# Performance work log

Measured on AMD Instinct MI355X. Metric: run time of the kernel, lower is better.

The kernel has to match this reference:

```python
import jax, jax.numpy as jnp
import numpy as np

B, GNN_DIM, TR_DIM, F = 16384, 512, 768, 1024


def setup_inputs() -> dict:
    key = jax.random.key(0)
    ks = jax.random.split(key, 16)
    s = 0.02
    return {
        "gnn_features": jax.random.normal(ks[0], (B, GNN_DIM), jnp.float32),
        "transformer_features": jax.random.normal(ks[1], (B, TR_DIM), jnp.float32),
        # gnn_projector / transformer_projector (torch Linear: y = x @ W.T + b)
        "Wg": jax.random.normal(ks[2], (F, GNN_DIM), jnp.float32) * s,
        "bg": jnp.zeros((F,), jnp.float32),
        "Wt": jax.random.normal(ks[3], (F, TR_DIM), jnp.float32) * s,
        "bt": jnp.zeros((F,), jnp.float32),
        # MultiheadAttention value-projection slice of in_proj_weight and out_proj.
        # With seq_len==1 the softmax over a single key is identically 1, so the
        # attention output is exactly out_proj(v_proj(key)); Q/K projections do
        # not affect the output (their gradients are exactly zero).
        "Wv": jax.random.normal(ks[4], (F, F), jnp.float32) * s,
        "bv": jnp.zeros((F,), jnp.float32),
        "Wo": jax.random.normal(ks[5], (F, F), jnp.float32) * s,
        "bo": jnp.zeros((F,), jnp.float32),
        # fusion_layers: Linear(2F -> F), GELU, Dropout(eval: identity), Linear(F -> F)
        "W1": jax.random.normal(ks[6], (F, 2 * F), jnp.float32) * s,
        "b1": jnp.zeros((F,), jnp.float32),
        "W2": jax.random.normal(ks[7], (F, F), jnp.float32) * s,
        "b2": jnp.zeros((F,), jnp.float32),
    }


def reference(gnn_features, transformer_features, Wg, bg, Wt, bt, Wv, bv, Wo, bo, W1, b1, W2, b2):
    # projections to fusion space  [B, F]
    gnn_proj = gnn_features @ Wg.T + bg
    tr_proj = transformer_features @ Wt.T + bt
    # degenerate single-token cross-attention: softmax over 1 key == 1, so
    # attn(q, k, v=k) = out_proj(v_proj(k)) regardless of the query.
    gnn_attended = (tr_proj @ Wv.T + bv) @ Wo.T + bo   # attention(gnn_seq, tr_seq, tr_seq)
    tr_attended = (gnn_proj @ Wv.T + bv) @ Wo.T + bo   # attention(tr_seq, gnn_seq, gnn_seq)
    combined = jnp.concatenate([gnn_attended, tr_attended], axis=-1)  # [B, 2F]
    h = jax.nn.gelu(combined @ W1.T + b1, approximate=False)          # exact GELU (torch default)
    fused = h @ W2.T + b2
    return fused + gnn_proj + tr_proj
```

## Files before the change

### kernel.cpp

```cpp
#include <hip/hip_runtime.h>
#include <cmath>

#define GAS __attribute__((address_space(1)))
#define LAS __attribute__((address_space(3)))

typedef __bf16 bf16x8 __attribute__((ext_vector_type(8)));
typedef float f32x4 __attribute__((ext_vector_type(4)));
typedef float f32x16 __attribute__((ext_vector_type(16)));

__device__ __forceinline__ void gload16(const void* g, void* l) {
    __builtin_amdgcn_global_load_lds((const GAS void*)g, (LAS void*)l, 16, 0, 0);
}

__global__ void k_prep(const float* __restrict__ gnn, const float* __restrict__ tr,
                       const float* __restrict__ Wo, const float* __restrict__ W1,
                       const float* __restrict__ W2, const float* __restrict__ Wg,
                       const float* __restrict__ Wt, const float* __restrict__ Wv,
                       __bf16* __restrict__ X, __bf16* __restrict__ W1ab,
                       __bf16* __restrict__ Wp, __bf16* __restrict__ Wv_b,
                       __bf16* __restrict__ WoT, __bf16* __restrict__ WgT,
                       __bf16* __restrict__ WtT) {
    __shared__ float t[32][33];
    int b = blockIdx.x;
    int tid = threadIdx.x;
    if (b < 12928) {
        const float* src; __bf16* dst; int sld, dld, base, c8;
        if (b < 4096)       { src=gnn;     sld=512;  dst=X+1024;         dld=2304; base=0;     c8=64; }
        else if (b < 10240) { src=tr;      sld=768;  dst=X+1536;         dld=2304; base=4096;  c8=96; }
        else if (b < 10752) { src=W1;      sld=2048; dst=W1ab;           dld=1024; base=10240; c8=128; }
        else if (b < 11264) { src=W1+1024; sld=2048; dst=W1ab+1024*1024; dld=1024; base=10752; c8=128; }
        else if (b < 11776) { src=W2;      sld=1024; dst=Wp;             dld=2304; base=11264; c8=128; }
        else if (b < 12032) { src=Wg;      sld=512;  dst=Wp+1024;        dld=2304; base=11776; c8=64; }
        else if (b < 12416) { src=Wt;      sld=768;  dst=Wp+1536;        dld=2304; base=12032; c8=96; }
        else                { src=Wv;      sld=1024; dst=Wv_b;           dld=1024; base=12416; c8=128; }
        int idx = (b - base) * 256 + tid;
        int r = idx / c8;
        int c = (idx - r * c8) << 3;
        const float4* s = reinterpret_cast<const float4*>(src + (long)r * sld + c);
        float4 x0 = s[0], x1 = s[1];
        bf16x8 v;
        v[0]=(__bf16)x0.x; v[1]=(__bf16)x0.y; v[2]=(__bf16)x0.z; v[3]=(__bf16)x0.w;
        v[4]=(__bf16)x1.x; v[5]=(__bf16)x1.y; v[6]=(__bf16)x1.z; v[7]=(__bf16)x1.w;
        *reinterpret_cast<bf16x8*>(dst + (long)r * dld + c) = v;
    } else {
        int bb = b - 12928;
        const float* src; __bf16* dst; int R, C, tile;
        if (bb < 1024)      { src=Wo; dst=WoT; R=1024; C=1024; tile=bb; }
        else if (bb < 1536) { src=Wg; dst=WgT; R=1024; C=512;  tile=bb-1024; }
        else                { src=Wt; dst=WtT; R=1024; C=768;  tile=bb-1536; }
        int tx_n = C >> 5;
        int c0 = (tile % tx_n) << 5, r0 = (tile / tx_n) << 5;
        int tx = tid & 31, ty = tid >> 5;
        #pragma unroll
        for (int i = 0; i < 32; i += 8)
            t[ty + i][tx] = src[(long)(r0 + ty + i) * C + c0 + tx];
        __syncthreads();
        #pragma unroll
        for (int i = 0; i < 32; i += 8)
            dst[(long)(c0 + ty + i) * R + r0 + tx] = (__bf16)t[tx][ty + i];
    }
}

__global__ void k_bias1(const float* __restrict__ Wo, const float* __restrict__ bv,
                        const float* __restrict__ bo, const float* __restrict__ Wv,
                        const float* __restrict__ bt, const float* __restrict__ bg,
                        float* __restrict__ b_att, float* __restrict__ vb_t,
                        float* __restrict__ vb_g) {
    int b = blockIdx.x;
    const float* mat; const float* vec; float* dst; int i; bool addbo = false;
    if (b < 1024)      { mat = Wo; vec = bv; dst = b_att; i = b;        addbo = true; }
    else if (b < 2048) { mat = Wv; vec = bt; dst = vb_t;  i = b - 1024; }
    else               { mat = Wv; vec = bg; dst = vb_g;  i = b - 2048; }
    float s = 0.f;
    for (int k = threadIdx.x; k < 1024; k += 256) s += mat[(long)i * 1024 + k] * vec[k];
    __shared__ float red[256];
    red[threadIdx.x] = s;
    __syncthreads();
    for (int off = 128; off > 0; off >>= 1) {
        if (threadIdx.x < off) red[threadIdx.x] += red[threadIdx.x + off];
        __syncthreads();
    }
    if (threadIdx.x == 0) dst[i] = red[0] + (addbo ? bo[i] : 0.f);
}

__global__ void k_bias_z2(const float* __restrict__ W1, const float* __restrict__ b_att,
                          const float* __restrict__ b1, const __bf16* __restrict__ U12,
                          const float* __restrict__ vb_t, const float* __restrict__ vb_g,
                          const float* __restrict__ bt, const float* __restrict__ bg,
                          const float* __restrict__ b2,
                          float* __restrict__ bz2, float* __restrict__ b_out) {
    int i = blockIdx.x;
    float s = 0.f;
    for (int k = threadIdx.x; k < 1024; k += 256) {
        s += (W1[(long)i * 2048 + k] + W1[(long)i * 2048 + 1024 + k]) * b_att[k];
        s += (float)U12[(long)i * 1024 + k] * vb_t[k];
        s += (float)U12[(long)(i + 1024) * 1024 + k] * vb_g[k];
    }
    __shared__ float red[256];
    red[threadIdx.x] = s;
    __syncthreads();
    for (int off = 128; off > 0; off >>= 1) {
        if (threadIdx.x < off) red[threadIdx.x] += red[threadIdx.x + off];
        __syncthreads();
    }
    if (threadIdx.x == 0) {
        bz2[i] = red[0] + b1[i];
        b_out[i] = b2[i] + bg[i] + bt[i];
    }
}

__device__ __forceinline__ void gemm64_body(
    const __bf16* __restrict__ A, int lda,
    const __bf16* __restrict__ B, int ldb,
    __bf16* __restrict__ C, int ldc,
    int K, int n_tiles, int bid) {
    constexpr int BM = 64, BN = 64, BK = 32;
    constexpr int MR = 2, NR = 2;
    __shared__ alignas(16) __bf16 As[2][BM][BK];
    __shared__ alignas(16) __bf16 Bs[2][BN][BK];

    const int tid = threadIdx.x;
    const int lane = tid & 63;
    const int wave = tid >> 6;
    const int bn = bid % n_tiles;
    const int bm = bid / n_tiles;
    const int m0 = bm * BM, n0 = bn * BN;

    const int rp_l = tid >> 2;
    const int sp = tid & 3;
    const int wr = (wave >> 1) * 32;
    const int wc = (wave & 1) * 32;
    const int fr = lane & 15;
    const int fb = (lane >> 4) << 4;

    f32x4 acc[MR][NR] = {};
    const int nk = K / BK;

    auto stage = [&](int buf, int kt) {
        int rl = (rp_l & ~1) | ((rp_l ^ (rp_l >> 2)) & 1);
        int sl = sp ^ (rl & 3);
        gload16(A + (long)(m0 + rl) * lda + kt * BK + sl * 8, (char*)&As[buf][0][0] + tid * 16);
        gload16(B + (long)(n0 + rl) * ldb + kt * BK + sl * 8, (char*)&Bs[buf][0][0] + tid * 16);
    };

    stage(0, 0);
    for (int kt = 0; kt < nk; ++kt) {
        const int buf = kt & 1;
        __syncthreads();
        if (kt + 1 < nk) stage(buf ^ 1, kt + 1);
        const char* abase = (const char*)&As[buf][0][0];
        const char* bbase = (const char*)&Bs[buf][0][0];
        bf16x8 af[MR], bfr[NR];
        #pragma unroll
        for (int m = 0; m < MR; ++m) {
            int r = wr + m * 16 + fr;
            af[m] = *(const bf16x8*)(abase + (((r << 6) + fb) ^ ((r & 7) << 4)));
        }
        #pragma unroll
        for (int n = 0; n < NR; ++n) {
            int r = wc + n * 16 + fr;
            bfr[n] = *(const bf16x8*)(bbase + (((r << 6) + fb) ^ ((r & 7) << 4)));
        }
        #pragma unroll
        for (int m = 0; m < MR; ++m)
            #pragma unroll
            for (int n = 0; n < NR; ++n)
                acc[m][n] = __builtin_amdgcn_mfma_f32_16x16x32_bf16(af[m], bfr[n], acc[m][n], 0, 0, 0);
    }

    const int r0 = (lane >> 4) << 2;
    #pragma unroll
    for (int n = 0; n < NR; ++n) {
        const int gc = n0 + wc + n * 16 + fr;
        #pragma unroll
        for (int m = 0; m < MR; ++m) {
            const long rbase = (long)(m0 + wr + m * 16 + r0);
            #pragma unroll
            for (int r = 0; r < 4; ++r)
                C[(rbase + r) * ldc + gc] = (__bf16)acc[m][n][r];
        }
    }
}

__global__ __launch_bounds__(256, 2) void k_gemmL1(
    const __bf16* __restrict__ W1ab, const __bf16* __restrict__ WoT,
    const __bf16* __restrict__ WtT, const __bf16* __restrict__ WgT,
    const __bf16* __restrict__ Wv_b, __bf16* __restrict__ U12,
    __bf16* __restrict__ VtT, __bf16* __restrict__ VgT) {
    int b = blockIdx.x;
    if (b < 512)      gemm64_body(W1ab, 1024, WoT, 1024, U12, 1024, 1024, 16, b);
    else if (b < 704) gemm64_body(WtT, 1024, Wv_b, 1024, VtT, 1024, 1024, 16, b - 512);
    else              gemm64_body(WgT, 1024, Wv_b, 1024, VgT, 1024, 1024, 16, b - 704);
}

__global__ __launch_bounds__(256, 2) void k_gemmL2(
    const __bf16* __restrict__ U12, const __bf16* __restrict__ VtT,
    const __bf16* __restrict__ VgT, __bf16* __restrict__ M1) {
    int b = blockIdx.x;
    if (b < 192) gemm64_body(U12, 1024, VtT, 1024, M1 + 512, 1280, 1024, 12, b);
    else         gemm64_body(U12 + 1024 * 1024, 1024, VgT, 1024, M1, 1280, 1024, 8, b - 192);
}

template <int MODE>
__device__ __forceinline__ void gemm8_body(
    const __bf16* __restrict__ A, int lda,
    const __bf16* __restrict__ B, int ldb,
    void* __restrict__ Cv, int ldc,
    const float* __restrict__ bias,
    int K, int n_tiles) {
    __shared__ char lds[131072];

    const int tid = threadIdx.x;
    const int lane = tid & 63;
    const int wave = tid >> 6;
    const int wm = wave >> 2;
    const int wn = wave & 3;

    int bid = blockIdx.x;
    const int nwg = gridDim.x;
    if ((nwg & 7) == 0) bid = (bid & 7) * (nwg >> 3) + (bid >> 3);
    const int bn = bid % n_tiles;
    const int bm = bid / n_tiles;
    const int m0 = bm * 256, n0 = bn * 256;

    const int rowA = ((tid >> 7) << 4) + (tid & 15);
    const int colA = (((tid >> 6) & 1) << 5) + (((tid >> 4) & 3) << 3);
    const int rowB = ((tid >> 6) << 4) + (tid & 15);
    const int colB = (((tid >> 4) & 3) << 3);
    const __bf16* Ag = A + (long)(m0 + rowA) * lda + colA;
    const __bf16* Bg = B + (long)(n0 + rowB) * ldb + colB;
    const int tid16 = tid * 16;

    const int laneA = ((lane >> 4) & 1) * 2048 + (lane >> 5) * 256 + (lane & 15) * 16;
    const int laneB = ((lane >> 4) & 1) * 1024 + (lane >> 5) * 256 + (lane & 15) * 16;
    const int bnh = wn >> 1;
    const int bno = (wn & 1) * 4096;

    f32x16 acc[4][2] = {};
    bf16x8 af[2][2];
    bf16x8 bfr[2][2][2];

    const int nk = K >> 6;
    const int NI = nk >> 1;

#define STAGE_A(PAR, KT, MH, QH) \
    gload16(Ag + (long)(KT) * 64 + (long)((MH) * 128 + (QH) * 64) * lda, \
            lds + (PAR) * 32768 + (MH) * 16384 + (QH) * 8192 + tid16)
#define STAGE_B(PAR, KT, NH, KK) \
    gload16(Bg + (long)(KT) * 64 + (KK) * 32 + (long)((NH) * 128) * ldb, \
            lds + 65536 + (PAR) * 32768 + (NH) * 16384 + (KK) * 8192 + tid16)
#define VMC8 asm volatile("s_waitcnt vmcnt(8)" ::: "memory")
#define VMC6 asm volatile("s_waitcnt vmcnt(6)" ::: "memory")
#define VMC0 asm volatile("s_waitcnt vmcnt(0)" ::: "memory")
#define BAR  __builtin_amdgcn_s_barrier()
#define RD_A32(PAR, QH, KK) { \
        const char* a_ = lds + (PAR) * 32768 + wm * 16384 + (QH) * 8192 + (KK) * 1024; \
        _Pragma("unroll") \
        for (int fm_ = 0; fm_ < 2; ++fm_) { \
            _Pragma("unroll") \
            for (int h_ = 0; h_ < 2; ++h_) \
                af[fm_][h_] = *(const bf16x8*)(a_ + fm_ * 4096 + h_ * 512 + laneA); } }
#define RD_B32(KK, PAR) { \
        const char* b_ = lds + 65536 + (PAR) * 32768 + bnh * 16384 + (KK) * 8192 + bno; \
        _Pragma("unroll") \
        for (int fn_ = 0; fn_ < 2; ++fn_) { \
            _Pragma("unroll") \
            for (int h_ = 0; h_ < 2; ++h_) \
                bfr[KK][h_][fn_] = *(const bf16x8*)(b_ + fn_ * 2048 + h_ * 512 + laneB); } }
#define MFMA8(QH, KK) { \
        __builtin_amdgcn_s_setprio(1); \
        _Pragma("unroll") \
        for (int h_ = 0; h_ < 2; ++h_) { \
            _Pragma("unroll") \
            for (int fm_ = 0; fm_ < 2; ++fm_) { \
                _Pragma("unroll") \
                for (int fn_ = 0; fn_ < 2; ++fn_) \
                    acc[(QH) * 2 + fm_][fn_] = __builtin_amdgcn_mfma_f32_32x32x16_bf16( \
                        af[fm_][h_], bfr[KK][h_][fn_], acc[(QH) * 2 + fm_][fn_], 0, 0, 0); } } \
        __builtin_amdgcn_s_setprio(0); }

    STAGE_A(0, 0, 0, 0); STAGE_A(0, 0, 1, 0);
    STAGE_B(0, 0, 0, 0); STAGE_B(0, 0, 1, 0);
    STAGE_A(0, 0, 0, 1); STAGE_A(0, 0, 1, 1);
    STAGE_B(0, 0, 0, 1); STAGE_B(0, 0, 1, 1);
    STAGE_A(1, 1, 0, 0); STAGE_A(1, 1, 1, 0);
    STAGE_B(1, 1, 0, 0); STAGE_B(1, 1, 1, 0);

    for (int I = 0; I < NI; ++I) {
        const int t = 2 * I;
        const bool nl = (I + 1 < NI);
        VMC8;
        STAGE_A(1, t + 1, 0, 1); STAGE_A(1, t + 1, 1, 1);
        BAR; RD_B32(0, 0); RD_A32(0, 0, 0); MFMA8(0, 0); BAR;
        VMC6;
        STAGE_B(1, t + 1, 0, 1); STAGE_B(1, t + 1, 1, 1);
        BAR; RD_B32(1, 0); RD_A32(0, 0, 1); MFMA8(0, 1); BAR;
        if (nl) { STAGE_A(0, t + 2, 0, 0); STAGE_A(0, t + 2, 1, 0); } else { VMC0; }
        BAR; RD_A32(0, 1, 0); MFMA8(1, 0); BAR;
        if (nl) { STAGE_B(0, t + 2, 0, 0); STAGE_B(0, t + 2, 1, 0); }
        BAR; RD_A32(0, 1, 1); MFMA8(1, 1); BAR;
        VMC8;
        if (nl) { STAGE_A(0, t + 2, 0, 1); STAGE_A(0, t + 2, 1, 1); }
        BAR; RD_B32(0, 1); RD_A32(1, 0, 0); MFMA8(0, 0); BAR;
        VMC6;
        if (nl) { STAGE_B(0, t + 2, 0, 1); STAGE_B(0, t + 2, 1, 1); }
        BAR; RD_B32(1, 1); RD_A32(1, 0, 1); MFMA8(0, 1); BAR;
        if (nl) { STAGE_A(1, t + 3, 0, 0); STAGE_A(1, t + 3, 1, 0); }
        BAR; RD_A32(1, 1, 0); MFMA8(1, 0); BAR;
        if (nl) { STAGE_B(1, t + 3, 0, 0); STAGE_B(1, t + 3, 1, 0); }
        BAR; RD_A32(1, 1, 1); MFMA8(1, 1); BAR;
    }
#undef MFMA8
#undef RD_B32
#undef RD_A32
#undef BAR
#undef VMC0
#undef VMC6
#undef VMC8
#undef STAGE_B
#undef STAGE_A

    char* scr = lds + wave * 16384;
    const int col32 = lane & 31;
    const int rb5 = (lane >> 5) << 2;
    float bval[2];
    bval[0] = bias ? bias[n0 + wn * 64 + col32] : 0.0f;
    bval[1] = bias ? bias[n0 + wn * 64 + 32 + col32] : 0.0f;

    #pragma unroll
    for (int FM = 0; FM < 4; ++FM) {
        #pragma unroll
        for (int fn_ = 0; fn_ < 2; ++fn_) {
            #pragma unroll
            for (int rg = 0; rg < 16; ++rg) {
                float v = acc[FM][fn_][rg] + bval[fn_];
                if (MODE == 1) {
                    float u = v * (0.7978845608f + 0.0356774081f * v * v);
                    float e = __expf(-2.0f * fabsf(u));
                    float th = (1.0f - e) / (1.0f + e);
                    th = copysignf(th, u);
                    v = 0.5f * v * (1.0f + th);
                }
                int srow = (rg & 3) + ((rg >> 2) << 3) + rb5;
                *(float*)(scr + srow * 272 + (fn_ * 32 + col32) * 4) = v;
            }
        }
        asm volatile("s_waitcnt lgkmcnt(0)" ::: "memory");
        if (MODE == 2) {
            #pragma unroll
            for (int rep = 0; rep < 8; ++rep) {
                int row = rep * 4 + (lane >> 4);
                f32x4 val = *(const f32x4*)(scr + row * 272 + (lane & 15) * 16);
                long grow = (long)(m0 + wm * 128 + FM * 32 + row);
                *(f32x4*)&((float*)Cv)[grow * ldc + n0 + wn * 64 + (lane & 15) * 4] = val;
            }
        } else {
            #pragma unroll
            for (int rep = 0; rep < 4; ++rep) {
                int row = rep * 8 + (lane >> 3);
                f32x4 v0 = *(const f32x4*)(scr + row * 272 + (lane & 7) * 32);
                f32x4 v1 = *(const f32x4*)(scr + row * 272 + (lane & 7) * 32 + 16);
                bf16x8 o;
                o[0] = (__bf16)v0[0]; o[1] = (__bf16)v0[1]; o[2] = (__bf16)v0[2]; o[3] = (__bf16)v0[3];
                o[4] = (__bf16)v1[0]; o[5] = (__bf16)v1[1]; o[6] = (__bf16)v1[2]; o[7] = (__bf16)v1[3];
                long grow = (long)(m0 + wm * 128 + FM * 32 + row);
                *(bf16x8*)&((__bf16*)Cv)[grow * ldc + n0 + wn * 64 + (lane & 7) * 8] = o;
            }
        }
        asm volatile("s_waitcnt lgkmcnt(0)" ::: "memory");
    }
}

__global__ __launch_bounds__(512, 2) void k_g256_gelu(
    const __bf16* __restrict__ A, int lda, const __bf16* __restrict__ B, int ldb,
    void* __restrict__ Cv, int ldc, const float* __restrict__ bias, int K, int n_tiles) {
    gemm8_body<1>(A, lda, B, ldb, Cv, ldc, bias, K, n_tiles);
}
__global__ __launch_bounds__(512, 2) void k_g256_out(
    const __bf16* __restrict__ A, int lda, const __bf16* __restrict__ B, int ldb,
    void* __restrict__ Cv, int ldc, const float* __restrict__ bias, int K, int n_tiles) {
    gemm8_body<2>(A, lda, B, ldb, Cv, ldc, bias, K, n_tiles);
}

extern "C" void kernel_launch(void* const* d_in, const int* in_sizes, int n_in,
                              void* d_out, int out_size, void* d_ws, size_t ws_size,
                              hipStream_t stream) {
    constexpr int Bsz = 16384, F = 1024, GD = 512, TD = 768;
    constexpr int XLD = F + GD + TD;

    const float* gnn = (const float*)d_in[0];
    const float* tr  = (const float*)d_in[1];
    const float* Wg  = (const float*)d_in[2];
    const float* bg  = (const float*)d_in[3];
    const float* Wt  = (const float*)d_in[4];
    const float* bt  = (const float*)d_in[5];
    const float* Wv  = (const float*)d_in[6];
    const float* bv  = (const float*)d_in[7];
    const float* Wo  = (const float*)d_in[8];
    const float* bo  = (const float*)d_in[9];
    const float* W1  = (const float*)d_in[10];
    const float* b1  = (const float*)d_in[11];
    const float* W2  = (const float*)d_in[12];
    const float* b2  = (const float*)d_in[13];
    float* out = (float*)d_out;

    char* w = (char*)d_ws;
    auto alloc = [&](size_t bytes) {
        char* p = w;
        w += (bytes + 255) & ~(size_t)255;
        return p;
    };
    __bf16* X    = (__bf16*)alloc((size_t)Bsz * XLD * 2);
    __bf16* M1   = (__bf16*)alloc((size_t)F * (GD + TD) * 2);
    __bf16* Wp   = (__bf16*)alloc((size_t)F * XLD * 2);
    __bf16* W1ab = (__bf16*)alloc((size_t)2 * F * F * 2);
    __bf16* Wv_b = (__bf16*)alloc((size_t)F * F * 2);
    __bf16* WoT  = (__bf16*)alloc((size_t)F * F * 2);
    __bf16* WgT  = (__bf16*)alloc((size_t)GD * F * 2);
    __bf16* WtT  = (__bf16*)alloc((size_t)TD * F * 2);
    __bf16* U12  = (__bf16*)alloc((size_t)2 * F * F * 2);
    __bf16* VtT  = (__bf16*)alloc((size_t)TD * F * 2);
    __bf16* VgT  = (__bf16*)alloc((size_t)GD * F * 2);
    float* b_att = (float*)alloc(F * 4);
    float* vb_t  = (float*)alloc(F * 4);
    float* vb_g  = (float*)alloc(F * 4);
    float* bz2   = (float*)alloc(F * 4);
    float* b_out = (float*)alloc(F * 4);
    if ((size_t)(w - (char*)d_ws) > ws_size) return;

    dim3 b256(256);

    k_prep<<<dim3(15232), b256, 0, stream>>>(gnn, tr, Wo, W1, W2, Wg, Wt, Wv,
                                             X, W1ab, Wp, Wv_b, WoT, WgT, WtT);
    k_bias1<<<dim3(3072), b256, 0, stream>>>(Wo, bv, bo, Wv, bt, bg, b_att, vb_t, vb_g);

    k_gemmL1<<<dim3(832), b256, 0, stream>>>(W1ab, WoT, WtT, WgT, Wv_b, U12, VtT, VgT);

    k_bias_z2<<<dim3(F), b256, 0, stream>>>(W1, b_att, b1, U12, vb_t, vb_g, bt, bg, b2,
                                            bz2, b_out);

    k_gemmL2<<<dim3(320), b256, 0, stream>>>(U12, VtT, VgT, M1);

    k_g256_gelu<<<dim3((Bsz / 256) * (F / 256)), dim3(512), 0, stream>>>(
        X + F, XLD, M1, GD + TD, X, XLD, bz2, GD + TD, F / 256);

    k_g256_out<<<dim3((Bsz / 256) * (F / 256)), dim3(512), 0, stream>>>(
        X, XLD, Wp, XLD, out, F, b_out, XLD, F / 256);
}
```

Baseline: 217.2 us.

## Double-buffer A fragments and prefetch LDS reads one MFMA phase ahead

Adds a second register set for the A fragments so the LDS reads for the next MFMA phase are issued before the barrier and the current MFMA block. The vmcnt waits are retuned (VMC6/VMC4) and sched_barrier pins keep the compiler from reordering the reads. This targets LDS read latency that sat exposed before each MFMA group. In exchange it uses more VGPRs and changes the barrier and wait ordering, which risks reading LDS data that is not ready or losing occupancy.

```diff
diff --git a/kernel.cpp b/kernel.cpp
--- a/kernel.cpp
+++ b/kernel.cpp
@@ -237,7 +237,7 @@
     const int bno = (wn & 1) * 4096;
 
     f32x16 acc[4][2] = {};
-    bf16x8 af[2][2];
+    bf16x8 af[2][2][2];
     bf16x8 bfr[2][2][2];
 
     const int nk = K >> 6;
@@ -249,17 +249,18 @@
 #define STAGE_B(PAR, KT, NH, KK) \
     gload16(Bg + (long)(KT) * 64 + (KK) * 32 + (long)((NH) * 128) * ldb, \
             lds + 65536 + (PAR) * 32768 + (NH) * 16384 + (KK) * 8192 + tid16)
-#define VMC8 asm volatile("s_waitcnt vmcnt(8)" ::: "memory")
 #define VMC6 asm volatile("s_waitcnt vmcnt(6)" ::: "memory")
+#define VMC4 asm volatile("s_waitcnt vmcnt(4)" ::: "memory")
 #define VMC0 asm volatile("s_waitcnt vmcnt(0)" ::: "memory")
 #define BAR  __builtin_amdgcn_s_barrier()
-#define RD_A32(PAR, QH, KK) { \
+#define PIN  __builtin_amdgcn_sched_barrier(0)
+#define RD_A32(S, PAR, QH, KK) { \
         const char* a_ = lds + (PAR) * 32768 + wm * 16384 + (QH) * 8192 + (KK) * 1024; \
         _Pragma("unroll") \
         for (int fm_ = 0; fm_ < 2; ++fm_) { \
             _Pragma("unroll") \
             for (int h_ = 0; h_ < 2; ++h_) \
-                af[fm_][h_] = *(const bf16x8*)(a_ + fm_ * 4096 + h_ * 512 + laneA); } }
+                af[S][fm_][h_] = *(const bf16x8*)(a_ + fm_ * 4096 + h_ * 512 + laneA); } }
 #define RD_B32(KK, PAR) { \
         const char* b_ = lds + 65536 + (PAR) * 32768 + bnh * 16384 + (KK) * 8192 + bno; \
         _Pragma("unroll") \
@@ -267,7 +268,7 @@
             _Pragma("unroll") \
             for (int h_ = 0; h_ < 2; ++h_) \
                 bfr[KK][h_][fn_] = *(const bf16x8*)(b_ + fn_ * 2048 + h_ * 512 + laneB); } }
-#define MFMA8(QH, KK) { \
+#define MFMA8(S, QH, KK) { \
         __builtin_amdgcn_s_setprio(1); \
         _Pragma("unroll") \
         for (int h_ = 0; h_ < 2; ++h_) { \
@@ -276,7 +277,7 @@
                 _Pragma("unroll") \
                 for (int fn_ = 0; fn_ < 2; ++fn_) \
                     acc[(QH) * 2 + fm_][fn_] = __builtin_amdgcn_mfma_f32_32x32x16_bf16( \
-                        af[fm_][h_], bfr[KK][h_][fn_], acc[(QH) * 2 + fm_][fn_], 0, 0, 0); } } \
+                        af[S][fm_][h_], bfr[KK][h_][fn_], acc[(QH) * 2 + fm_][fn_], 0, 0, 0); } } \
         __builtin_amdgcn_s_setprio(0); }
 
     STAGE_A(0, 0, 0, 0); STAGE_A(0, 0, 1, 0);
@@ -285,38 +286,49 @@
     STAGE_B(0, 0, 0, 1); STAGE_B(0, 0, 1, 1);
     STAGE_A(1, 1, 0, 0); STAGE_A(1, 1, 1, 0);
     STAGE_B(1, 1, 0, 0); STAGE_B(1, 1, 1, 0);
+    VMC4;
+    BAR;
+    RD_B32(0, 0); RD_A32(0, 0, 0, 0);
 
     for (int I = 0; I < NI; ++I) {
         const int t = 2 * I;
         const bool nl = (I + 1 < NI);
-        VMC8;
         STAGE_A(1, t + 1, 0, 1); STAGE_A(1, t + 1, 1, 1);
-        BAR; RD_B32(0, 0); RD_A32(0, 0, 0); MFMA8(0, 0); BAR;
-        VMC6;
+        RD_B32(1, 0); RD_A32(1, 0, 0, 1); PIN;
+        BAR; MFMA8(0, 0, 0); BAR;
         STAGE_B(1, t + 1, 0, 1); STAGE_B(1, t + 1, 1, 1);
-        BAR; RD_B32(1, 0); RD_A32(0, 0, 1); MFMA8(0, 1); BAR;
-        if (nl) { STAGE_A(0, t + 2, 0, 0); STAGE_A(0, t + 2, 1, 0); } else { VMC0; }
-        BAR; RD_A32(0, 1, 0); MFMA8(1, 0); BAR;
-        if (nl) { STAGE_B(0, t + 2, 0, 0); STAGE_B(0, t + 2, 1, 0); }
-        BAR; RD_A32(0, 1, 1); MFMA8(1, 1); BAR;
-        VMC8;
+        RD_A32(0, 0, 1, 0); PIN;
+        BAR; MFMA8(1, 0, 1); BAR;
+        if (nl) { STAGE_A(0, t + 2, 0, 0); STAGE_A(0, t + 2, 1, 0); VMC6; } else { VMC0; }
+        RD_A32(1, 0, 1, 1); PIN;
+        BAR; MFMA8(0, 1, 0); BAR;
+        if (nl) { STAGE_B(0, t + 2, 0, 0); STAGE_B(0, t + 2, 1, 0); VMC4; }
+        RD_B32(0, 1); RD_A32(0, 1, 0, 0); PIN;
+        BAR; MFMA8(1, 1, 1); BAR;
         if (nl) { STAGE_A(0, t + 2, 0, 1); STAGE_A(0, t + 2, 1, 1); }
-        BAR; RD_B32(0, 1); RD_A32(1, 0, 0); MFMA8(0, 0); BAR;
-        VMC6;
+        RD_B32(1, 1); RD_A32(1, 1, 0, 1); PIN;
+        BAR; MFMA8(0, 0, 0); BAR;
         if (nl) { STAGE_B(0, t + 2, 0, 1); STAGE_B(0, t + 2, 1, 1); }
-        BAR; RD_B32(1, 1); RD_A32(1, 0, 1); MFMA8(0, 1); BAR;
-        if (nl) { STAGE_A(1, t + 3, 0, 0); STAGE_A(1, t + 3, 1, 0); }
-        BAR; RD_A32(1, 1, 0); MFMA8(1, 0); BAR;
-        if (nl) { STAGE_B(1, t + 3, 0, 0); STAGE_B(1, t + 3, 1, 0); }
-        BAR; RD_A32(1, 1, 1); MFMA8(1, 1); BAR;
+        RD_A32(0, 1, 1, 0); PIN;
+        BAR; MFMA8(1, 0, 1); BAR;
+        if (nl) { STAGE_A(1, t + 3, 0, 0); STAGE_A(1, t + 3, 1, 0); VMC6; }
+        RD_A32(1, 1, 1, 1); PIN;
+        BAR; MFMA8(0, 1, 0); BAR;
+        if (nl) {
+            STAGE_B(1, t + 3, 0, 0); STAGE_B(1, t + 3, 1, 0); VMC4;
+            RD_B32(0, 0); RD_A32(0, 0, 0, 0);
+        }
+        PIN;
+        BAR; MFMA8(1, 1, 1); BAR;
     }
 #undef MFMA8
 #undef RD_B32
 #undef RD_A32
+#undef PIN
 #undef BAR
 #undef VMC0
+#undef VMC4
 #undef VMC6
-#undef VMC8
 #undef STAGE_B
 #undef STAGE_A
 
```

After: 217.3 us. No clear change (+0.1%).

## Reorder GEMM main loop to issue LDS reads before global stages

Applied to the files above, without the earlier changes.

Restructures the software-pipelined GEMM main loop so that LDS fragment reads are issued before the next global-to-LDS stage loads and an explicit lgkmcnt wait precedes each MFMA block. The prologue now stages both B halves of the second tile and waits once on vmcnt before entering the loop. Stage ordering and the vmcnt wait points move so that B halves are prefetched earlier. The aim is to hide LDS read latency behind global load issue and relax memory waits, at the cost of a more fragile hand-tuned wait-count schedule.

```diff
diff --git a/kernel.cpp b/kernel.cpp
--- a/kernel.cpp
+++ b/kernel.cpp
@@ -31,7 +31,7 @@
         else if (b < 11264) { src=W1+1024; sld=2048; dst=W1ab+1024*1024; dld=1024; base=10752; c8=128; }
         else if (b < 11776) { src=W2;      sld=1024; dst=Wp;             dld=2304; base=11264; c8=128; }
         else if (b < 12032) { src=Wg;      sld=512;  dst=Wp+1024;        dld=2304; base=11776; c8=64; }
-        else if (b < 12416) { src=Wt;      sld=768;  dst=Wp+1536;        dld=2304; base=12032; c8=96; }
+        else if (b < 12416) { src=Wt;      sld=768;  dst=Wp+1536;       dld=2304; base=12032; c8=96; }
         else                { src=Wv;      sld=1024; dst=Wv_b;           dld=1024; base=12416; c8=128; }
         int idx = (b - base) * 256 + tid;
         int r = idx / c8;
@@ -249,10 +249,10 @@
 #define STAGE_B(PAR, KT, NH, KK) \
     gload16(Bg + (long)(KT) * 64 + (KK) * 32 + (long)((NH) * 128) * ldb, \
             lds + 65536 + (PAR) * 32768 + (NH) * 16384 + (KK) * 8192 + tid16)
-#define VMC8 asm volatile("s_waitcnt vmcnt(8)" ::: "memory")
 #define VMC6 asm volatile("s_waitcnt vmcnt(6)" ::: "memory")
 #define VMC0 asm volatile("s_waitcnt vmcnt(0)" ::: "memory")
 #define BAR  __builtin_amdgcn_s_barrier()
+#define LGKM0 asm volatile("s_waitcnt lgkmcnt(0)" ::: "memory")
 #define RD_A32(PAR, QH, KK) { \
         const char* a_ = lds + (PAR) * 32768 + wm * 16384 + (QH) * 8192 + (KK) * 1024; \
         _Pragma("unroll") \
@@ -281,42 +281,49 @@
 
     STAGE_A(0, 0, 0, 0); STAGE_A(0, 0, 1, 0);
     STAGE_B(0, 0, 0, 0); STAGE_B(0, 0, 1, 0);
+    STAGE_B(0, 0, 0, 1); STAGE_B(0, 0, 1, 1);
     STAGE_A(0, 0, 0, 1); STAGE_A(0, 0, 1, 1);
-    STAGE_B(0, 0, 0, 1); STAGE_B(0, 0, 1, 1);
     STAGE_A(1, 1, 0, 0); STAGE_A(1, 1, 1, 0);
     STAGE_B(1, 1, 0, 0); STAGE_B(1, 1, 1, 0);
+    STAGE_B(1, 1, 0, 1); STAGE_B(1, 1, 1, 1);
+    VMC6;
+    BAR;
 
     for (int I = 0; I < NI; ++I) {
         const int t = 2 * I;
         const bool nl = (I + 1 < NI);
-        VMC8;
+        RD_B32(0, 0); RD_A32(0, 0, 0);
         STAGE_A(1, t + 1, 0, 1); STAGE_A(1, t + 1, 1, 1);
-        BAR; RD_B32(0, 0); RD_A32(0, 0, 0); MFMA8(0, 0); BAR;
-        VMC6;
-        STAGE_B(1, t + 1, 0, 1); STAGE_B(1, t + 1, 1, 1);
-        BAR; RD_B32(1, 0); RD_A32(0, 0, 1); MFMA8(0, 1); BAR;
-        if (nl) { STAGE_A(0, t + 2, 0, 0); STAGE_A(0, t + 2, 1, 0); } else { VMC0; }
-        BAR; RD_A32(0, 1, 0); MFMA8(1, 0); BAR;
+        BAR; LGKM0; MFMA8(0, 0); BAR;
+        RD_B32(1, 0); RD_A32(0, 0, 1);
         if (nl) { STAGE_B(0, t + 2, 0, 0); STAGE_B(0, t + 2, 1, 0); }
-        BAR; RD_A32(0, 1, 1); MFMA8(1, 1); BAR;
-        VMC8;
+        BAR; LGKM0; MFMA8(0, 1); BAR;
+        RD_A32(0, 1, 0);
+        if (nl) { STAGE_A(0, t + 2, 0, 0); STAGE_A(0, t + 2, 1, 0); }
+        BAR; LGKM0; MFMA8(1, 0); BAR;
+        RD_A32(0, 1, 1);
+        if (nl) { STAGE_B(0, t + 2, 0, 1); STAGE_B(0, t + 2, 1, 1); VMC6; } else { VMC0; }
+        BAR; LGKM0; MFMA8(1, 1); BAR;
+        RD_B32(0, 1); RD_A32(1, 0, 0);
         if (nl) { STAGE_A(0, t + 2, 0, 1); STAGE_A(0, t + 2, 1, 1); }
-        BAR; RD_B32(0, 1); RD_A32(1, 0, 0); MFMA8(0, 0); BAR;
-        VMC6;
-        if (nl) { STAGE_B(0, t + 2, 0, 1); STAGE_B(0, t + 2, 1, 1); }
-        BAR; RD_B32(1, 1); RD_A32(1, 0, 1); MFMA8(0, 1); BAR;
+        BAR; LGKM0; MFMA8(0, 0); BAR;
+        RD_B32(1, 1); RD_A32(1, 0, 1);
+        if (nl) { STAGE_B(1, t + 3, 0, 0); STAGE_B(1, t + 3, 1, 0); }
+        BAR; LGKM0; MFMA8(0, 1); BAR;
+        RD_A32(1, 1, 0);
         if (nl) { STAGE_A(1, t + 3, 0, 0); STAGE_A(1, t + 3, 1, 0); }
-        BAR; RD_A32(1, 1, 0); MFMA8(1, 0); BAR;
-        if (nl) { STAGE_B(1, t + 3, 0, 0); STAGE_B(1, t + 3, 1, 0); }
-        BAR; RD_A32(1, 1, 1); MFMA8(1, 1); BAR;
+        BAR; LGKM0; MFMA8(1, 0); BAR;
+        RD_A32(1, 1, 1);
+        if (nl) { STAGE_B(1, t + 3, 0, 1); STAGE_B(1, t + 3, 1, 1); VMC6; }
+        BAR; LGKM0; MFMA8(1, 1); BAR;
     }
 #undef MFMA8
 #undef RD_B32
 #undef RD_A32
+#undef LGKM0
 #undef BAR
 #undef VMC0
 #undef VMC6
-#undef VMC8
 #undef STAGE_B
 #undef STAGE_A
 
```

Result: no change. 217.1 us, median of 2 (-0.0%).
